# Kernel optimization log

Measured on AMD Instinct MI355X. Metric: run time of the kernel, lower is better.

## Reference

```python
import jax, jax.numpy as jnp
import numpy as np

C = 64
CR = C // 8  # reduced channels for Q/K


def _conv1x1(x, W, b):
    # 1x1 conv == per-pixel linear over channels: x [b,c,h,w], W [o,c], b [o]
    return jnp.einsum('bchw,oc->bohw', x, W) + b[None, :, None, None]


def setup_inputs() -> dict:
    key = jax.random.key(0)
    ks = jax.random.split(key, 12)
    b, c, h, w = 8, C, 48, 48
    s = 1.0 / np.sqrt(c)
    inp = {
        'x1': jax.random.normal(ks[0], (b, c, h, w), jnp.float32),
        'x2': jax.random.normal(ks[1], (b, c, h, w), jnp.float32),
        'Wqk1': jax.random.normal(ks[2], (2 * CR, c), jnp.float32) * s,
        'bqk1': jnp.zeros((2 * CR,), jnp.float32),
        'Wqk2': jax.random.normal(ks[3], (2 * CR, c), jnp.float32) * s,
        'bqk2': jnp.zeros((2 * CR,), jnp.float32),
        'Wv1': jax.random.normal(ks[4], (c, c), jnp.float32) * s,
        'bv1': jnp.zeros((c,), jnp.float32),
        'Wv2': jax.random.normal(ks[5], (c, c), jnp.float32) * s,
        'bv2': jnp.zeros((c,), jnp.float32),
        'gamma': jnp.zeros((1,), jnp.float32) + 0.1,  # nonzero so output depends on attn
        'beta': jnp.zeros((1,), jnp.float32) + 0.1,
    }
    return inp


def reference(x1, x2, Wqk1, bqk1, Wqk2, bqk2, Wv1, bv1, Wv2, bv2, gamma, beta):
    b, c, h, w = x1.shape
    n = h * w
    qk1 = _conv1x1(x1, Wqk1, bqk1)
    qk2 = _conv1x1(x2, Wqk2, bqk2)
    q1, k1 = qk1[:, :CR], qk1[:, CR:]
    q2, k2 = qk2[:, :CR], qk2[:, CR:]
    # flatten spatial: [b, cr, n]
    q1 = q1.reshape(b, CR, n); k1 = k1.reshape(b, CR, n)
    q2 = q2.reshape(b, CR, n); k2 = k2.reshape(b, CR, n)
    v1 = _conv1x1(x1, Wv1, bv1).reshape(b, c, n)
    v2 = _conv1x1(x2, Wv2, bv2).reshape(b, c, n)
    # attn[b,i,j] = softmax_j( q[:, :, i] . k[:, :, j] )
    attn1 = jax.nn.softmax(jnp.einsum('bci,bcj->bij', q1, k1), axis=-1)
    attn2 = jax.nn.softmax(jnp.einsum('bci,bcj->bij', q2, k2), axis=-1)
    # out[:, :, j] = sum_i v[:, :, i] * attn[:, i, j]
    o1 = jnp.einsum('bci,bij->bcj', v1, attn2).reshape(b, c, h, w) * gamma + x1
    o2 = jnp.einsum('bci,bij->bcj', v2, attn1).reshape(b, c, h, w) * beta + x2
    return (o1, o2)
```

## Files before the change

### kernel.cpp

```cpp
#include <hip/hip_runtime.h>
#include <hip/hip_bf16.h>

#define NB   8
#define CCH  64
#define CR8  8
#define NPX  2304
#define BCN  (NB*CCH*NPX)
#define LOG2E 1.4426950408889634f

typedef short  short8   __attribute__((ext_vector_type(8)));
typedef unsigned short ushort8t __attribute__((ext_vector_type(8)));
typedef float  float4t  __attribute__((ext_vector_type(4)));
typedef float  float16t __attribute__((ext_vector_type(16)));

static __device__ __forceinline__ float fexp2(float x) {
    return __builtin_amdgcn_exp2f(x);
}
static __device__ __forceinline__ unsigned short bf16r(float f) {
    return (unsigned short)((__float_as_uint(f) + 0x8000u) >> 16);
}
static __device__ __forceinline__ unsigned int pack_bf16(float lo, float hi) {
    const unsigned int ul = __float_as_uint(lo) + 0x8000u;
    const unsigned int uh = __float_as_uint(hi) + 0x8000u;
    return __builtin_amdgcn_perm(uh, ul, 0x07060302u);
}
static __device__ __forceinline__ short8 pack8(const float* f) {
    union { unsigned int u[4]; short8 s; } r;
    #pragma unroll
    for (int j = 0; j < 4; j++) r.u[j] = pack_bf16(f[2*j], f[2*j+1]);
    return r.s;
}

#define WS_QB1 0
#define WS_KB1 (WS_QB1 + 147456)
#define WS_QB2 (WS_KB1 + 147456)
#define WS_KB2 (WS_QB2 + 147456)
#define WS_V1  (WS_KB2 + 147456)
#define WS_V2  (WS_V1 + BCN/2)
#define WS_PD  (WS_V2 + BCN/2)

__global__ __launch_bounds__(256) void proj_kernel(
    const float* __restrict__ x1, const float* __restrict__ x2,
    const float* __restrict__ Wqk1, const float* __restrict__ bqk1,
    const float* __restrict__ Wqk2, const float* __restrict__ bqk2,
    const float* __restrict__ Wv1,  const float* __restrict__ bv1,
    const float* __restrict__ Wv2,  const float* __restrict__ bv2,
    float* __restrict__ ws, float* __restrict__ out)
{
    const int t    = threadIdx.x;
    const int lane = t & 63;
    const int w    = t >> 6;
    const int n16  = lane & 15;
    const int c4   = lane >> 4;
    const int nt   = w & 1;
    const int mh   = w >> 1;
    const int b    = blockIdx.y;
    const int px   = blockIdx.x * 32 + nt * 16 + n16;

    const float* xsb[2];
    xsb[0] = x1 + ((size_t)b * CCH) * NPX + px;
    xsb[1] = x2 + ((size_t)b * CCH) * NPX + px;

    float xr[2][16];
    short8 bfrag[2][2];
    #pragma unroll
    for (int st = 0; st < 2; st++) {
        #pragma unroll
        for (int ch = 0; ch < 2; ch++) {
            #pragma unroll
            for (int j = 0; j < 8; j++)
                xr[st][ch * 8 + j] = xsb[st][(ch * 32 + c4 * 8 + j) * NPX];
            bfrag[st][ch] = pack8(&xr[st][ch * 8]);
        }
    }

    if (mh == 0) {
        #pragma unroll
        for (int st = 0; st < 2; st++) {
            float* outs = out + (st ? (size_t)BCN : 0);
            #pragma unroll
            for (int e = 0; e < 16; e++) {
                const int ch = (e >> 3) * 32 + c4 * 8 + (e & 7);
                outs[((size_t)b * CCH + ch) * NPX + px] = xr[st][e];
            }
        }
    }

    float4t acc[5];
    #pragma unroll
    for (int mt = 0; mt < 5; mt++) { acc[mt][0]=0.f; acc[mt][1]=0.f; acc[mt][2]=0.f; acc[mt][3]=0.f; }

    #pragma unroll
    for (int mt = 0; mt < 5; mt++) {
        const int mi  = mh * 5 + mt;
        const int isqk = (mi < 2);
        const int st  = isqk ? (mi & 1) : (mi >= 6);
        const float* Wb;
        int rowbase;
        if (isqk) { Wb = (mi == 0) ? Wqk1 : Wqk2; rowbase = 0; }
        else      { Wb = (mi >= 6) ? Wv2 : Wv1; rowbase = (mi - (mi >= 6 ? 6 : 2)) * 16; }
        const float* wrow = Wb + (size_t)(rowbase + n16) * 64 + c4 * 8;

        const short8 bf0 = st ? bfrag[1][0] : bfrag[0][0];
        const short8 bf1 = st ? bfrag[1][1] : bfrag[0][1];

        #pragma unroll
        for (int ch = 0; ch < 2; ch++) {
            float fa[8];
            const float4 a0 = *(const float4*)(wrow + ch * 32);
            const float4 a1 = *(const float4*)(wrow + ch * 32 + 4);
            fa[0] = a0.x; fa[1] = a0.y; fa[2] = a0.z; fa[3] = a0.w;
            fa[4] = a1.x; fa[5] = a1.y; fa[6] = a1.z; fa[7] = a1.w;
            acc[mt] = __builtin_amdgcn_mfma_f32_16x16x32_bf16(
                pack8(fa), ch ? bf1 : bf0, acc[mt], 0, 0, 0);
        }
    }

    #pragma unroll
    for (int mt = 0; mt < 5; mt++) {
        const int mi = mh * 5 + mt;
        if (mi < 2) {
            const int st = mi & 1;
            const float* bqk = st ? bqk2 : bqk1;
            unsigned short* qb = (unsigned short*)(ws + (st ? WS_QB2 : WS_QB1));
            unsigned short* kb = (unsigned short*)(ws + (st ? WS_KB2 : WS_KB1));
            const size_t rbase = (size_t)(b * NPX + px) * 16;
            #pragma unroll
            for (int r = 0; r < 4; r++) {
                const int oc = c4 * 4 + r;
                const float val = acc[mt][r] + bqk[oc];
                if (oc < 8)
                    qb[rbase + oc] = bf16r(val * LOG2E);
                else
                    kb[rbase + (oc - 8)] = bf16r(val);
            }
            ushort8t zq, zk;
            #pragma unroll
            for (int e = 0; e < 8; e++) { zq[e] = 0; zk[e] = 0; }
            zk[0] = 0x3F80; zk[1] = 0x3F80;
            if (c4 == 0) *(ushort8t*)(qb + rbase + 8) = zq;
            if (c4 == 2) *(ushort8t*)(kb + rbase + 8) = zk;
        } else {
            const int st = (mi >= 6);
            const int vt_ = mi - (st ? 6 : 2);
            const float* bv = st ? bv2 : bv1;
            unsigned short* v = (unsigned short*)(ws + (st ? WS_V2 : WS_V1));
            #pragma unroll
            for (int r = 0; r < 4; r++) {
                const int oc = vt_ * 16 + c4 * 4 + r;
                const float val = acc[mt][r] + bv[oc];
                v[((size_t)b * CCH + oc) * NPX + px] = bf16r(val);
            }
        }
    }
}

__global__ __launch_bounds__(256) void stats_kernel(float* __restrict__ ws)
{
    const int t  = threadIdx.x;
    const int w  = t >> 6;
    const int n  = t & 31;
    const int h  = (t & 63) >> 5;
    const int jsb = blockIdx.x;
    const int iq  = blockIdx.y;
    const int ab  = blockIdx.z;
    const int b   = ab & 7;
    const int a   = ab >> 3;

    const unsigned short* qb = (const unsigned short*)(ws + (a ? WS_QB2 : WS_QB1));
    const unsigned short* kb = (const unsigned short*)(ws + (a ? WS_KB2 : WS_KB1));
    float* pd = ws + WS_PD;

    __shared__ float red[4][288];

    const int j = jsb * 128 + w * 32 + n;
    const short8 kfrag = *(const short8*)(kb + (size_t)(b * NPX + j) * 16 + h * 8);

    const unsigned short* qp = qb + (size_t)(b * NPX + iq * 288 + n) * 16 + h * 8;
    short8 qf = *(const short8*)qp;

    for (int ib = 0; ib < 9; ib++) {
        qp += 512;
        short8 qn = qf;
        if (ib + 1 < 9) qn = *(const short8*)qp;
        float16t acc = {};
        acc = __builtin_amdgcn_mfma_f32_32x32x16_bf16(kfrag, qf, acc, 0, 0, 0);
        float s0 = 0.f, s1 = 0.f, s2 = 0.f, s3 = 0.f;
        #pragma unroll
        for (int r = 0; r < 4; r++) {
            s0 += fexp2(acc[4 * r + 0]);
            s1 += fexp2(acc[4 * r + 1]);
            s2 += fexp2(acc[4 * r + 2]);
            s3 += fexp2(acc[4 * r + 3]);
        }
        float ssum = (s0 + s1) + (s2 + s3);
        ssum += __shfl_xor(ssum, 32);
        if (h == 0) red[w][ib * 32 + n] = ssum;
        qf = qn;
    }
    __syncthreads();
    for (int idx = t; idx < 288; idx += 256)
        pd[((size_t)ab * 18 + jsb) * NPX + iq * 288 + idx] =
            red[0][idx] + red[1][idx] + red[2][idx] + red[3][idx];
}

__global__ __launch_bounds__(256) void merge_fold(float* __restrict__ ws)
{
    const float* pd = ws + WS_PD;
    const int t  = threadIdx.x;
    const int il = t & 63;
    const int pg = t >> 6;
    const int i  = blockIdx.x * 64 + il;
    const int ab = blockIdx.y;
    const int b  = ab & 7;
    const int a  = ab >> 3;

    __shared__ float red[4][64];

    const float* pb = pd + (size_t)ab * 18 * NPX + i;
    float d = 0.f;
    #pragma unroll
    for (int c = pg; c < 18; c += 4)
        d += pb[(size_t)c * NPX];
    red[pg][il] = d;
    __syncthreads();

    if (t < 64) {
        const float dt = (red[0][t] + red[1][t]) + (red[2][t] + red[3][t]);
        const float m = -__log2f(dt);
        const unsigned short mh = bf16r(m);
        __hip_bfloat16 hb; *(unsigned short*)&hb = mh;
        const unsigned short ml = bf16r(m - __bfloat162float(hb));
        unsigned short* qb = (unsigned short*)(ws + (a ? WS_QB2 : WS_QB1));
        const size_t rbase = (size_t)(b * NPX + blockIdx.x * 64 + t) * 16;
        qb[rbase + 8] = mh;
        qb[rbase + 9] = ml;
    }
}

__global__ __launch_bounds__(256) void out_kernel(
    const float* __restrict__ gamma, const float* __restrict__ beta,
    const float* __restrict__ ws, float* __restrict__ out)
{
    const int t  = threadIdx.x;
    const int jt = blockIdx.x;
    const int b  = blockIdx.y;
    const int z  = blockIdx.z;
    const int o  = z >> 2;
    const int ihalf = z & 3;

    const int a = o ? 0 : 1;
    const unsigned short* qb = (const unsigned short*)(ws + (a ? WS_QB2 : WS_QB1));
    const unsigned short* kb = (const unsigned short*)(ws + (a ? WS_KB2 : WS_KB1));
    const unsigned short* v  = (const unsigned short*)(ws + (o ? WS_V2 : WS_V1));
    const float  scale = o ? beta[0] : gamma[0];

    __shared__ unsigned short vt[64][72];
    __shared__ unsigned short pt[64][72];

    const int j0   = jt * 64;
    const int lane = t & 63;
    const int w    = t >> 6;
    const int n    = lane & 31;
    const int h    = lane >> 5;
    const int jh   = w & 1;
    const int ihq  = w >> 1;
    const int cbase = 32 * (w & 1);
    const int jbase = 32 * (w >> 1);

    const short8 kfrag = *(const short8*)(kb + (size_t)(b * NPX + j0 + 32 * jh + n) * 16 + h * 8);

    const int c0 = t >> 3, s80 = (t & 7) * 8;
    const int c1 = (t + 256) >> 3, s81 = ((t + 256) & 7) * 8;

    const int ibase = ihalf * 576;
    const unsigned short* vp0 = v + ((size_t)b * CCH + c0) * NPX + ibase + s80;
    const unsigned short* vp1 = v + ((size_t)b * CCH + c1) * NPX + ibase + s81;
    const unsigned short* qp  = qb + (size_t)(b * NPX + ibase + 32 * ihq + n) * 16 + h * 8;

    float4 vpre0 = *(const float4*)vp0;
    float4 vpre1 = *(const float4*)vp1;
    short8 qpre  = *(const short8*)qp;

    float16t oacc = {};

    for (int it = 0; it < 9; it++) {
        vp0 += 64; vp1 += 64; qp += 64 * 16;
        float4 vn0 = vpre0, vn1 = vpre1;
        short8 qn = qpre;
        if (it + 1 < 9) {
            vn0 = *(const float4*)vp0;
            vn1 = *(const float4*)vp1;
            qn  = *(const short8*)qp;
        }

        __syncthreads();

        *(float4*)&vt[c0][s80] = vpre0;
        *(float4*)&vt[c1][s81] = vpre1;

        float16t sc = {};
        sc = __builtin_amdgcn_mfma_f32_32x32x16_bf16(qpre, kfrag, sc, 0, 0, 0);

        #pragma unroll
        for (int gq = 0; gq < 4; gq++) {
            const int ibl = 32 * ihq + 8 * gq + 4 * h;
            uint2 pk;
            pk.x = pack_bf16(fexp2(sc[gq * 4 + 0]), fexp2(sc[gq * 4 + 1]));
            pk.y = pack_bf16(fexp2(sc[gq * 4 + 2]), fexp2(sc[gq * 4 + 3]));
            *(uint2*)&pt[32 * jh + n][ibl] = pk;
        }
        __syncthreads();

        #pragma unroll
        for (int kk = 0; kk < 4; kk++) {
            const short8 afrag = *(const short8*)&vt[cbase + n][kk * 16 + h * 8];
            const short8 bfrag = *(const short8*)&pt[jbase + n][kk * 16 + h * 8];
            oacc = __builtin_amdgcn_mfma_f32_32x32x16_bf16(afrag, bfrag, oacc, 0, 0, 0);
        }

        vpre0 = vn0; vpre1 = vn1; qpre = qn;
    }

    float* outp = out + (o ? BCN : 0) + (b * CCH + cbase) * NPX + j0 + jbase + n;
    #pragma unroll
    for (int r = 0; r < 16; r++) {
        const int row = (r & 3) + 8 * (r >> 2) + 4 * h;
        atomicAdd(outp + row * NPX, oacc[r] * scale);
    }
}

extern "C" void kernel_launch(void* const* d_in, const int* in_sizes, int n_in,
                              void* d_out, int out_size, void* d_ws, size_t ws_size,
                              hipStream_t stream)
{
    const float* x1   = (const float*)d_in[0];
    const float* x2   = (const float*)d_in[1];
    const float* Wqk1 = (const float*)d_in[2];
    const float* bqk1 = (const float*)d_in[3];
    const float* Wqk2 = (const float*)d_in[4];
    const float* bqk2 = (const float*)d_in[5];
    const float* Wv1  = (const float*)d_in[6];
    const float* bv1  = (const float*)d_in[7];
    const float* Wv2  = (const float*)d_in[8];
    const float* bv2  = (const float*)d_in[9];
    const float* gamma = (const float*)d_in[10];
    const float* beta  = (const float*)d_in[11];
    float* out = (float*)d_out;
    float* ws  = (float*)d_ws;

    proj_kernel<<<dim3(72, 8), 256, 0, stream>>>(
        x1, x2, Wqk1, bqk1, Wqk2, bqk2, Wv1, bv1, Wv2, bv2, ws, out);
    stats_kernel<<<dim3(18, 8, 16), 256, 0, stream>>>(ws);
    merge_fold<<<dim3(36, 16), 256, 0, stream>>>(ws);
    out_kernel<<<dim3(36, 8, 8), 256, 0, stream>>>(gamma, beta, ws, out);
}
```

Measured before the change: 146.0 us.

## Keep softmax probabilities in registers via permlane32 swap instead of LDS

The output kernel now gives each wave its own 32-column j tile and computes scores for all 64 i rows of each step. The exp'd probabilities are repacked into MFMA B fragments in registers with v_permlane32_swap instead of being staged through a shared pt buffer. This removes one LDS buffer and its reads and writes. Each wave now covers all 64 channels with two accumulators, and the grid is halved along j. The cost is more registers per wave and half as many blocks, so occupancy may drop.

```diff
diff --git a/kernel.cpp b/kernel.cpp
--- a/kernel.cpp
+++ b/kernel.cpp
@@ -29,6 +29,29 @@
     #pragma unroll
     for (int j = 0; j < 4; j++) r.u[j] = pack_bf16(f[2*j], f[2*j+1]);
     return r.s;
+}
+
+static __device__ __forceinline__ void build_bfrag(const float16t sc, short8* bf) {
+    unsigned int d[4][2];
+    #pragma unroll
+    for (int q = 0; q < 4; q++) {
+        #pragma unroll
+        for (int m = 0; m < 2; m++)
+            d[q][m] = pack_bf16(fexp2(sc[4*q + 2*m]), fexp2(sc[4*q + 2*m + 1]));
+    }
+    #pragma unroll
+    for (int kp = 0; kp < 2; kp++) {
+        union { unsigned int u[4]; short8 s; } r;
+        #pragma unroll
+        for (int m = 0; m < 2; m++) {
+            unsigned int x = d[2*kp][m];
+            unsigned int y = d[2*kp + 1][m];
+            asm("v_permlane32_swap_b32 %0, %1" : "+v"(x), "+v"(y));
+            r.u[m]     = x;
+            r.u[2 + m] = y;
+        }
+        bf[kp] = r.s;
+    }
 }
 
 #define WS_QB1 0
@@ -256,19 +279,15 @@
     const float  scale = o ? beta[0] : gamma[0];
 
     __shared__ unsigned short vt[64][72];
-    __shared__ unsigned short pt[64][72];
-
-    const int j0   = jt * 64;
+
     const int lane = t & 63;
     const int w    = t >> 6;
     const int n    = lane & 31;
     const int h    = lane >> 5;
-    const int jh   = w & 1;
-    const int ihq  = w >> 1;
-    const int cbase = 32 * (w & 1);
-    const int jbase = 32 * (w >> 1);
-
-    const short8 kfrag = *(const short8*)(kb + (size_t)(b * NPX + j0 + 32 * jh + n) * 16 + h * 8);
+
+    const int j0 = jt * 128 + w * 32;
+
+    const short8 kfrag = *(const short8*)(kb + (size_t)(b * NPX + j0 + n) * 16 + h * 8);
 
     const int c0 = t >> 3, s80 = (t & 7) * 8;
     const int c1 = (t + 256) >> 3, s81 = ((t + 256) & 7) * 8;
@@ -276,22 +295,24 @@
     const int ibase = ihalf * 576;
     const unsigned short* vp0 = v + ((size_t)b * CCH + c0) * NPX + ibase + s80;
     const unsigned short* vp1 = v + ((size_t)b * CCH + c1) * NPX + ibase + s81;
-    const unsigned short* qp  = qb + (size_t)(b * NPX + ibase + 32 * ihq + n) * 16 + h * 8;
+    const unsigned short* qp  = qb + (size_t)(b * NPX + ibase + n) * 16 + h * 8;
 
     float4 vpre0 = *(const float4*)vp0;
     float4 vpre1 = *(const float4*)vp1;
-    short8 qpre  = *(const short8*)qp;
-
-    float16t oacc = {};
+    short8 qpre0 = *(const short8*)qp;
+    short8 qpre1 = *(const short8*)(qp + 32 * 16);
+
+    float16t oacc0 = {}, oacc1 = {};
 
     for (int it = 0; it < 9; it++) {
         vp0 += 64; vp1 += 64; qp += 64 * 16;
         float4 vn0 = vpre0, vn1 = vpre1;
-        short8 qn = qpre;
+        short8 qn0 = qpre0, qn1 = qpre1;
         if (it + 1 < 9) {
             vn0 = *(const float4*)vp0;
             vn1 = *(const float4*)vp1;
-            qn  = *(const short8*)qp;
+            qn0 = *(const short8*)qp;
+            qn1 = *(const short8*)(qp + 32 * 16);
         }
 
         __syncthreads();
@@ -299,34 +320,44 @@
         *(float4*)&vt[c0][s80] = vpre0;
         *(float4*)&vt[c1][s81] = vpre1;
 
-        float16t sc = {};
-        sc = __builtin_amdgcn_mfma_f32_32x32x16_bf16(qpre, kfrag, sc, 0, 0, 0);
-
-        #pragma unroll
-        for (int gq = 0; gq < 4; gq++) {
-            const int ibl = 32 * ihq + 8 * gq + 4 * h;
-            uint2 pk;
-            pk.x = pack_bf16(fexp2(sc[gq * 4 + 0]), fexp2(sc[gq * 4 + 1]));
-            pk.y = pack_bf16(fexp2(sc[gq * 4 + 2]), fexp2(sc[gq * 4 + 3]));
-            *(uint2*)&pt[32 * jh + n][ibl] = pk;
-        }
+        float16t sc0 = {}, sc1 = {};
+        sc0 = __builtin_amdgcn_mfma_f32_32x32x16_bf16(qpre0, kfrag, sc0, 0, 0, 0);
+        sc1 = __builtin_amdgcn_mfma_f32_32x32x16_bf16(qpre1, kfrag, sc1, 0, 0, 0);
+
+        short8 bfA[2], bfB[2];
+        build_bfrag(sc0, bfA);
+        build_bfrag(sc1, bfB);
+
         __syncthreads();
 
-        #pragma unroll
-        for (int kk = 0; kk < 4; kk++) {
-            const short8 afrag = *(const short8*)&vt[cbase + n][kk * 16 + h * 8];
-            const short8 bfrag = *(const short8*)&pt[jbase + n][kk * 16 + h * 8];
-            oacc = __builtin_amdgcn_mfma_f32_32x32x16_bf16(afrag, bfrag, oacc, 0, 0, 0);
-        }
-
-        vpre0 = vn0; vpre1 = vn1; qpre = qn;
-    }
-
-    float* outp = out + (o ? BCN : 0) + (b * CCH + cbase) * NPX + j0 + jbase + n;
+        {
+            const short8 a0 = *(const short8*)&vt[n][0 * 16 + h * 8];
+            const short8 a1 = *(const short8*)&vt[32 + n][0 * 16 + h * 8];
+            oacc0 = __builtin_amdgcn_mfma_f32_32x32x16_bf16(a0, bfA[0], oacc0, 0, 0, 0);
+            oacc1 = __builtin_amdgcn_mfma_f32_32x32x16_bf16(a1, bfA[0], oacc1, 0, 0, 0);
+            const short8 a2 = *(const short8*)&vt[n][1 * 16 + h * 8];
+            const short8 a3 = *(const short8*)&vt[32 + n][1 * 16 + h * 8];
+            oacc0 = __builtin_amdgcn_mfma_f32_32x32x16_bf16(a2, bfA[1], oacc0, 0, 0, 0);
+            oacc1 = __builtin_amdgcn_mfma_f32_32x32x16_bf16(a3, bfA[1], oacc1, 0, 0, 0);
+            const short8 a4 = *(const short8*)&vt[n][2 * 16 + h * 8];
+            const short8 a5 = *(const short8*)&vt[32 + n][2 * 16 + h * 8];
+            oacc0 = __builtin_amdgcn_mfma_f32_32x32x16_bf16(a4, bfB[0], oacc0, 0, 0, 0);
+            oacc1 = __builtin_amdgcn_mfma_f32_32x32x16_bf16(a5, bfB[0], oacc1, 0, 0, 0);
+            const short8 a6 = *(const short8*)&vt[n][3 * 16 + h * 8];
+            const short8 a7 = *(const short8*)&vt[32 + n][3 * 16 + h * 8];
+            oacc0 = __builtin_amdgcn_mfma_f32_32x32x16_bf16(a6, bfB[1], oacc0, 0, 0, 0);
+            oacc1 = __builtin_amdgcn_mfma_f32_32x32x16_bf16(a7, bfB[1], oacc1, 0, 0, 0);
+        }
+
+        vpre0 = vn0; vpre1 = vn1; qpre0 = qn0; qpre1 = qn1;
+    }
+
+    float* outp = out + (o ? BCN : 0) + (b * CCH) * NPX + j0 + n;
     #pragma unroll
     for (int r = 0; r < 16; r++) {
         const int row = (r & 3) + 8 * (r >> 2) + 4 * h;
-        atomicAdd(outp + row * NPX, oacc[r] * scale);
+        atomicAdd(outp + row * NPX, oacc0[r] * scale);
+        atomicAdd(outp + (32 + row) * NPX, oacc1[r] * scale);
     }
 }
 
@@ -353,5 +384,5 @@
         x1, x2, Wqk1, bqk1, Wqk2, bqk2, Wv1, bv1, Wv2, bv2, ws, out);
     stats_kernel<<<dim3(18, 8, 16), 256, 0, stream>>>(ws);
     merge_fold<<<dim3(36, 16), 256, 0, stream>>>(ws);
-    out_kernel<<<dim3(36, 8, 8), 256, 0, stream>>>(gamma, beta, ws, out);
-}
+    out_kernel<<<dim3(18, 8, 8), 256, 0, stream>>>(gamma, beta, ws, out);
+}
```

New measurement: 151.2 us. 1.04x slower.
